# Performance work log

Hardware: AMD Instinct MI355X
Metric: run time of the kernel (lower is better)

## Reference

```python
import jax, jax.numpy as jnp
import numpy as np

N, K, F, H, C = 16384, 16, 3, 64, 10


def setup_inputs() -> dict:
    key = jax.random.key(0)
    ks = jax.random.split(key, 6)
    pos = jax.random.normal(ks[0], (N, F), jnp.float32)
    batch = jnp.zeros((N,), jnp.int32)  # single graph
    W1 = jax.random.normal(ks[1], (2 * F, H), jnp.float32) * 0.1
    b1 = jnp.zeros((H,), jnp.float32)
    W2 = jax.random.normal(ks[2], (2 * H, H), jnp.float32) * 0.1
    b2 = jnp.zeros((H,), jnp.float32)
    Wc = jax.random.normal(ks[3], (H, C), jnp.float32) * 0.1
    bc = jnp.zeros((C,), jnp.float32)
    return {"pos": pos, "batch": batch, "W1": W1, "b1": b1,
            "W2": W2, "b2": b2, "Wc": Wc, "bc": bc}


def knn_graph(pos, k):
    # brute-force knn with self-loops (loop=True): self has distance 0
    sq = jnp.sum(pos * pos, axis=1)
    d = sq[:, None] + sq[None, :] - 2.0 * (pos @ pos.T)  # [N, N]
    _, idx = jax.lax.top_k(-d, k)  # [N, k] nearest neighbor indices (incl. self)
    return idx


def edge_conv(x, idx, W, b):
    # message for edge j->i: Linear(concat(x_i, x_j - x_i)); aggregate by max over neighbors
    n, k = idx.shape
    xi = x[:, None, :]               # [N, 1, F]
    xj = x[idx]                      # [N, k, F]
    msg = jnp.concatenate([jnp.broadcast_to(xi, (n, k, x.shape[1])), xj - xi], axis=-1)
    m = msg @ W + b                  # [N, k, H]
    return jnp.max(m, axis=1)        # [N, H]


def reference(pos, batch, W1, b1, W2, b2, Wc, bc):
    idx = knn_graph(pos, K)
    h = jax.nn.relu(edge_conv(pos, idx, W1, b1))
    h = jax.nn.relu(edge_conv(h, idx, W2, b2))
    g = jax.ops.segment_max(h, batch, num_segments=1)  # global max pool -> [1, H]
    return g @ Wc + bc
```

## Files before the change

### kernel.cpp

```cpp
#include <hip/hip_runtime.h>

#define NPTS 16384
#define KNN 16
#define HID 64
#define NCLS 10

#define WPB 4
#define QPB 8
#define CPW (NPTS / WPB)
#define SCAP 128

__device__ __forceinline__ float distm2(float qx, float qy, float qz, float4 c) {
    return fmaf(qx, c.x, fmaf(qy, c.y, fmaf(qz, c.z, c.w)));
}

__device__ __forceinline__ unsigned long long dkey(float v, int j) {
    unsigned u = __float_as_uint(v);
    u = (u & 0x80000000u) ? ~u : (u | 0x80000000u);
    return ((unsigned long long)u << 32) | (unsigned)j;
}

__device__ __forceinline__ unsigned long long shfl_xor_u64(unsigned long long x, int m) {
    unsigned hi = (unsigned)__shfl_xor((int)(x >> 32), m, 64);
    unsigned lo = (unsigned)__shfl_xor((int)(x & 0xffffffffu), m, 64);
    return ((unsigned long long)hi << 32) | lo;
}

__device__ __forceinline__ void wave_top16_16(unsigned long long (&key)[16], int lane,
                                              int q, int* __restrict__ idx) {
    int outj = 0x7fffffff;
    for (int r = 0; r < 16; ++r) {
        unsigned long long gm = key[0];
#pragma unroll
        for (int s = 1; s < 16; ++s) gm = key[s] < gm ? key[s] : gm;
#pragma unroll
        for (int st = 1; st < 64; st <<= 1) {
            unsigned long long o = shfl_xor_u64(gm, st);
            gm = o < gm ? o : gm;
        }
        if (lane == r) outj = (int)(gm & 0xffffffffu);
#pragma unroll
        for (int s = 0; s < 16; ++s)
            if (key[s] == gm) key[s] = ~0ull;
    }
    if (lane < 16) idx[q * KNN + lane] = outj;
}

__global__ void prep_kernel(const float* __restrict__ pos, float4* __restrict__ pos4,
                            float4* __restrict__ pm2) {
    int i = blockIdx.x * 256 + threadIdx.x;
    if (i < NPTS) {
        float x = pos[3 * i], y = pos[3 * i + 1], z = pos[3 * i + 2];
        float sq = fmaf(x, x, fmaf(y, y, z * z));
        pos4[i] = make_float4(x, y, z, sq);
        pm2[i] = make_float4(-2.f * x, -2.f * y, -2.f * z, sq);
    }
}

__global__ __launch_bounds__(256) void knn_kernel(const float4* __restrict__ pos4,
                                                  const float4* __restrict__ pm2,
                                                  int* __restrict__ idx) {
    __shared__ unsigned long long keys[QPB][SCAP];
    __shared__ int knt[QPB];
    __shared__ float smin[QPB][WPB][16];
    int tid = threadIdx.x;
    int lane = tid & 63;
    int w = tid >> 6;
    int qb = blockIdx.x * QPB;
    float qx[QPB], qy[QPB], qz[QPB];
#pragma unroll
    for (int i = 0; i < QPB; ++i) {
        float4 t = pos4[qb + i];
        qx[i] = t.x; qy[i] = t.y; qz[i] = t.z;
    }
    int base = w * CPW;

    float mn[QPB];
#pragma unroll
    for (int i = 0; i < QPB; ++i) mn[i] = INFINITY;
    {
        float4 c0 = pm2[base + lane],       c1 = pm2[base + 64 + lane];
        float4 d0 = pm2[base + 128 + lane], d1 = pm2[base + 192 + lane];
        for (int cb = base; cb < base + CPW; cb += 128) {
#pragma unroll
            for (int i = 0; i < QPB; ++i) {
                float va = distm2(qx[i], qy[i], qz[i], c0);
                float vb = distm2(qx[i], qy[i], qz[i], c1);
                mn[i] = fminf(mn[i], fminf(va, vb));
            }
            c0 = d0; c1 = d1;
            d0 = pm2[cb + 256 + lane];
            d1 = pm2[cb + 320 + lane];
        }
    }
#pragma unroll
    for (int i = 0; i < QPB; ++i) {
        float m = mn[i];
        m = fminf(m, __shfl_xor(m, 16, 64));
        m = fminf(m, __shfl_xor(m, 32, 64));
        if (lane < 16) smin[i][w][lane] = m;
    }
    if (tid < QPB) knt[tid] = 0;
    __syncthreads();

    float tq[QPB];
#pragma unroll
    for (int i = 0; i < QPB; ++i) {
        int s = lane & 15;
        float m = fminf(fminf(smin[i][0][s], smin[i][1][s]),
                        fminf(smin[i][2][s], smin[i][3][s]));
        m = fmaxf(m, __shfl_xor(m, 1, 64));
        m = fmaxf(m, __shfl_xor(m, 2, 64));
        m = fmaxf(m, __shfl_xor(m, 4, 64));
        m = fmaxf(m, __shfl_xor(m, 8, 64));
        tq[i] = m;
    }

    {
        float4 c0 = pm2[base + lane],       c1 = pm2[base + 64 + lane];
        float4 d0 = pm2[base + 128 + lane], d1 = pm2[base + 192 + lane];
        for (int cb = base; cb < base + CPW; cb += 128) {
            int j0 = cb + lane, j1 = cb + 64 + lane;
#pragma unroll
            for (int i = 0; i < QPB; ++i) {
                float va = distm2(qx[i], qy[i], qz[i], c0);
                float vb = distm2(qx[i], qy[i], qz[i], c1);
                if (fminf(va, vb) <= tq[i]) {
                    if (va <= tq[i]) { int s = atomicAdd(&knt[i], 1); if (s < SCAP) keys[i][s] = dkey(va, j0); }
                    if (vb <= tq[i]) { int s = atomicAdd(&knt[i], 1); if (s < SCAP) keys[i][s] = dkey(vb, j1); }
                }
            }
            c0 = d0; c1 = d1;
            d0 = pm2[cb + 256 + lane];
            d1 = pm2[cb + 320 + lane];
        }
    }
    __syncthreads();

#pragma unroll
    for (int e = 0; e < 2; ++e) {
        int qi = w * 2 + e;
        int q = qb + qi;
        int ntot = knt[qi];
        if (ntot <= SCAP) {
            unsigned long long k0 = (lane < ntot) ? keys[qi][lane] : ~0ull;
            unsigned long long k1 = (lane + 64 < ntot) ? keys[qi][lane + 64] : ~0ull;
            int r0 = 0, r1 = 0;
            for (int t = 0; t < ntot; ++t) {
                unsigned long long k = keys[qi][t];
                r0 += (int)(k < k0);
                r1 += (int)(k < k1);
            }
            if (lane < ntot && r0 < KNN) idx[q * KNN + r0] = (int)(k0 & 0xffffffffu);
            if (lane + 64 < ntot && r1 < KNN) idx[q * KNN + r1] = (int)(k1 & 0xffffffffu);
        } else {
            float tqq = tq[qi];
            unsigned long long key[16];
#pragma unroll
            for (int u = 0; u < 16; ++u) key[u] = ~0ull;
            for (int j = lane; j < NPTS; j += 64) {
                float v = distm2(qx[qi], qy[qi], qz[qi], pm2[j]);
                unsigned long long k = dkey(v, j);
                if (v <= tqq && k < key[15]) {
#pragma unroll
                    for (int s = 0; s < 16; ++s) {
                        unsigned long long a = k < key[s] ? k : key[s];
                        unsigned long long b = k < key[s] ? key[s] : k;
                        key[s] = a;
                        k = b;
                    }
                }
            }
            wave_top16_16(key, lane, q, idx);
        }
    }
}

__global__ __launch_bounds__(256) void ec12_kernel(const float4* __restrict__ pos4,
                                                   const int* __restrict__ idx,
                                                   const float* __restrict__ W1,
                                                   const float* __restrict__ b1,
                                                   const float* __restrict__ W2,
                                                   const float* __restrict__ b2,
                                                   float* __restrict__ C2,
                                                   float* __restrict__ Y2) {
    __shared__ float h1s[16][64];
    int t = threadIdx.x & 63;
    int w = threadIdx.x >> 6;
    int pb = blockIdx.x * 16 + w * 4;
    float w0 = W1[0 * HID + t], w1 = W1[1 * HID + t], w2 = W1[2 * HID + t];
    float v0 = W1[3 * HID + t], v1 = W1[4 * HID + t], v2 = W1[5 * HID + t];
    float bt1 = b1[t];
#pragma unroll
    for (int i = 0; i < 4; ++i) {
        int p = pb + i;
        float4 xi = pos4[p];
        float C = bt1 + xi.x * (w0 - v0) + xi.y * (w1 - v1) + xi.z * (w2 - v2);
        float m = -INFINITY;
#pragma unroll
        for (int k = 0; k < KNN; ++k) {
            int j = idx[p * KNN + k];
            float4 xj = pos4[j];
            m = fmaxf(m, fmaf(xj.x, v0, fmaf(xj.y, v1, xj.z * v2)));
        }
        h1s[w * 4 + i][t] = fmaxf(C + m, 0.f);
    }
    __syncthreads();
    float aa[4] = {0.f, 0.f, 0.f, 0.f};
    float ab[4] = {0.f, 0.f, 0.f, 0.f};
#pragma unroll 8
    for (int f = 0; f < 64; ++f) {
        float wa = W2[f * HID + t];
        float wb = W2[(64 + f) * HID + t];
#pragma unroll
        for (int i = 0; i < 4; ++i) {
            float h = h1s[w * 4 + i][f];
            aa[i] = fmaf(h, wa, aa[i]);
            ab[i] = fmaf(h, wb, ab[i]);
        }
    }
    float bt = b2[t];
#pragma unroll
    for (int i = 0; i < 4; ++i) {
        C2[(pb + i) * HID + t] = bt + aa[i] - ab[i];
        Y2[(pb + i) * HID + t] = ab[i];
    }
}

__global__ __launch_bounds__(256) void ec2_maxpool_kernel(const float* __restrict__ C2,
                                                          const float* __restrict__ Y2,
                                                          const int* __restrict__ idx,
                                                          float* __restrict__ gpartial) {
    int t = threadIdx.x & 63;
    int lp = threadIdx.x >> 6;
    int p = blockIdx.x * 4 + lp;
    float m = -INFINITY;
#pragma unroll
    for (int k = 0; k < KNN; ++k) {
        int j = idx[p * KNN + k];
        m = fmaxf(m, Y2[j * HID + t]);
    }
    float val = fmaxf(C2[p * HID + t] + m, 0.f);
    __shared__ float red[4][64];
    red[lp][t] = val;
    __syncthreads();
    if (lp == 0) {
        float g = fmaxf(fmaxf(red[0][t], red[1][t]), fmaxf(red[2][t], red[3][t]));
        gpartial[blockIdx.x * 64 + t] = g;
    }
}

__global__ __launch_bounds__(256) void greduce2_kernel(const float* __restrict__ gpartial,
                                                       float* __restrict__ gp2) {
    __shared__ float red[4][64];
    int f = threadIdx.x & 63;
    int w = threadIdx.x >> 6;
    int r0 = blockIdx.x * 16 + w * 4;
    float m = -INFINITY;
#pragma unroll
    for (int r = 0; r < 4; ++r) m = fmaxf(m, gpartial[(r0 + r) * 64 + f]);
    red[w][f] = m;
    __syncthreads();
    if (w == 0)
        gp2[blockIdx.x * 64 + f] =
            fmaxf(fmaxf(red[0][f], red[1][f]), fmaxf(red[2][f], red[3][f]));
}

__global__ __launch_bounds__(256) void tail2_kernel(const float* __restrict__ gp2,
                                                    const float* __restrict__ Wc,
                                                    const float* __restrict__ bc,
                                                    float* __restrict__ out) {
    __shared__ float red[4][64];
    __shared__ float g[64];
    int f = threadIdx.x & 63;
    int w = threadIdx.x >> 6;
    float m = -INFINITY;
    for (int i = w; i < 256; i += 4) m = fmaxf(m, gp2[i * 64 + f]);
    red[w][f] = m;
    __syncthreads();
    if (w == 0) g[f] = fmaxf(fmaxf(red[0][f], red[1][f]), fmaxf(red[2][f], red[3][f]));
    __syncthreads();
    if (threadIdx.x < NCLS) {
        float a = bc[threadIdx.x];
#pragma unroll
        for (int h = 0; h < HID; ++h) a = fmaf(g[h], Wc[h * NCLS + threadIdx.x], a);
        out[threadIdx.x] = a;
    }
}

extern "C" void kernel_launch(void* const* d_in, const int* in_sizes, int n_in,
                              void* d_out, int out_size, void* d_ws, size_t ws_size,
                              hipStream_t stream) {
    const float* pos = (const float*)d_in[0];
    const float* W1 = (const float*)d_in[2];
    const float* b1 = (const float*)d_in[3];
    const float* W2 = (const float*)d_in[4];
    const float* b2 = (const float*)d_in[5];
    const float* Wc = (const float*)d_in[6];
    const float* bc = (const float*)d_in[7];
    float* out = (float*)d_out;

    char* ws = (char*)d_ws;
    size_t o = 0;
    auto alloc = [&](size_t bytes) { size_t r = o; o += (bytes + 255) & ~size_t(255); return r; };
    size_t fm = (size_t)NPTS * HID * 4;
    size_t o_pos4 = alloc((size_t)NPTS * 16);
    size_t o_pm2 = alloc((size_t)(NPTS + 320) * 16);
    size_t o_idx = alloc((size_t)NPTS * KNN * 4);
    size_t o_C2 = alloc(fm);
    size_t o_Y2 = alloc(fm);
    size_t o_gp = alloc((size_t)(NPTS / 4) * HID * 4);
    size_t o_gp2 = alloc((size_t)256 * HID * 4);

    float4* pos4 = (float4*)(ws + o_pos4);
    float4* pm2 = (float4*)(ws + o_pm2);
    int* idx = (int*)(ws + o_idx);
    float* C2 = (float*)(ws + o_C2);
    float* Y2 = (float*)(ws + o_Y2);
    float* gp = (float*)(ws + o_gp);
    float* gp2 = (float*)(ws + o_gp2);

    hipMemsetAsync(pm2 + NPTS, 0, 320 * sizeof(float4), stream);

    prep_kernel<<<NPTS / 256, 256, 0, stream>>>(pos, pos4, pm2);
    knn_kernel<<<NPTS / QPB, 256, 0, stream>>>(pos4, pm2, idx);
    ec12_kernel<<<NPTS / 16, 256, 0, stream>>>(pos4, idx, W1, b1, W2, b2, C2, Y2);
    ec2_maxpool_kernel<<<NPTS / 4, 256, 0, stream>>>(C2, Y2, idx, gp);
    greduce2_kernel<<<256, 256, 0, stream>>>(gp, gp2);
    tail2_kernel<<<1, 256, 0, stream>>>(gp2, Wc, bc, out);
}
```

Measured before the change: 305.9 us.

## Double KNN queries per block, force uniform query regs, vectorize neighbor index loads

Raises queries per block from 8 to 16, so each candidate point loaded from memory is reused across twice as many queries and the launch needs half as many blocks. Query coordinates and thresholds are forced into scalar registers with readfirstlane. The rank-counting loop over the candidate list is unrolled by 8. Neighbor indices in the two edge-conv kernels are fetched as int4 vectors. The costs are more registers and shared memory per block, which can lower occupancy, and fewer blocks to spread across the GPU.

```diff
diff --git a/kernel.cpp b/kernel.cpp
--- a/kernel.cpp
+++ b/kernel.cpp
@@ -6,12 +6,16 @@
 #define NCLS 10
 
 #define WPB 4
-#define QPB 8
+#define QPB 16
 #define CPW (NPTS / WPB)
 #define SCAP 128
 
 __device__ __forceinline__ float distm2(float qx, float qy, float qz, float4 c) {
     return fmaf(qx, c.x, fmaf(qy, c.y, fmaf(qz, c.z, c.w)));
+}
+
+__device__ __forceinline__ float __frfl(float x) {
+    return __int_as_float(__builtin_amdgcn_readfirstlane(__float_as_int(x)));
 }
 
 __device__ __forceinline__ unsigned long long dkey(float v, int j) {
@@ -70,8 +74,8 @@
     float qx[QPB], qy[QPB], qz[QPB];
 #pragma unroll
     for (int i = 0; i < QPB; ++i) {
-        float4 t = pos4[qb + i];
-        qx[i] = t.x; qy[i] = t.y; qz[i] = t.z;
+        float4 t4 = pos4[qb + i];
+        qx[i] = __frfl(t4.x); qy[i] = __frfl(t4.y); qz[i] = __frfl(t4.z);
     }
     int base = w * CPW;
 
@@ -113,7 +117,7 @@
         m = fmaxf(m, __shfl_xor(m, 2, 64));
         m = fmaxf(m, __shfl_xor(m, 4, 64));
         m = fmaxf(m, __shfl_xor(m, 8, 64));
-        tq[i] = m;
+        tq[i] = __frfl(m);
     }
 
     {
@@ -138,15 +142,26 @@
     __syncthreads();
 
 #pragma unroll
-    for (int e = 0; e < 2; ++e) {
-        int qi = w * 2 + e;
+    for (int e = 0; e < 4; ++e) {
+        int qi = w * 4 + e;
         int q = qb + qi;
         int ntot = knt[qi];
         if (ntot <= SCAP) {
             unsigned long long k0 = (lane < ntot) ? keys[qi][lane] : ~0ull;
             unsigned long long k1 = (lane + 64 < ntot) ? keys[qi][lane + 64] : ~0ull;
             int r0 = 0, r1 = 0;
-            for (int t = 0; t < ntot; ++t) {
+            int t = 0;
+            for (; t + 8 <= ntot; t += 8) {
+                unsigned long long a0 = keys[qi][t + 0], a1 = keys[qi][t + 1];
+                unsigned long long a2 = keys[qi][t + 2], a3 = keys[qi][t + 3];
+                unsigned long long a4 = keys[qi][t + 4], a5 = keys[qi][t + 5];
+                unsigned long long a6 = keys[qi][t + 6], a7 = keys[qi][t + 7];
+                r0 += (int)(a0 < k0) + (int)(a1 < k0) + (int)(a2 < k0) + (int)(a3 < k0)
+                    + (int)(a4 < k0) + (int)(a5 < k0) + (int)(a6 < k0) + (int)(a7 < k0);
+                r1 += (int)(a0 < k1) + (int)(a1 < k1) + (int)(a2 < k1) + (int)(a3 < k1)
+                    + (int)(a4 < k1) + (int)(a5 < k1) + (int)(a6 < k1) + (int)(a7 < k1);
+            }
+            for (; t < ntot; ++t) {
                 unsigned long long k = keys[qi][t];
                 r0 += (int)(k < k0);
                 r1 += (int)(k < k1);
@@ -196,11 +211,14 @@
         int p = pb + i;
         float4 xi = pos4[p];
         float C = bt1 + xi.x * (w0 - v0) + xi.y * (w1 - v1) + xi.z * (w2 - v2);
+        const int4* ip = (const int4*)(idx + (size_t)p * KNN);
+        int4 n0 = ip[0], n1 = ip[1], n2 = ip[2], n3 = ip[3];
+        int jj[16] = {n0.x, n0.y, n0.z, n0.w, n1.x, n1.y, n1.z, n1.w,
+                      n2.x, n2.y, n2.z, n2.w, n3.x, n3.y, n3.z, n3.w};
         float m = -INFINITY;
 #pragma unroll
         for (int k = 0; k < KNN; ++k) {
-            int j = idx[p * KNN + k];
-            float4 xj = pos4[j];
+            float4 xj = pos4[jj[k]];
             m = fmaxf(m, fmaf(xj.x, v0, fmaf(xj.y, v1, xj.z * v2)));
         }
         h1s[w * 4 + i][t] = fmaxf(C + m, 0.f);
@@ -234,11 +252,14 @@
     int t = threadIdx.x & 63;
     int lp = threadIdx.x >> 6;
     int p = blockIdx.x * 4 + lp;
+    const int4* ip = (const int4*)(idx + (size_t)p * KNN);
+    int4 n0 = ip[0], n1 = ip[1], n2 = ip[2], n3 = ip[3];
+    int jj[16] = {n0.x, n0.y, n0.z, n0.w, n1.x, n1.y, n1.z, n1.w,
+                  n2.x, n2.y, n2.z, n2.w, n3.x, n3.y, n3.z, n3.w};
     float m = -INFINITY;
 #pragma unroll
     for (int k = 0; k < KNN; ++k) {
-        int j = idx[p * KNN + k];
-        m = fmaxf(m, Y2[j * HID + t]);
+        m = fmaxf(m, Y2[jj[k] * HID + t]);
     }
     float val = fmaxf(C2[p * HID + t] + m, 0.f);
     __shared__ float red[4][64];
```

Result: slower. 315.6 us (+3.2%).
